# Kernel tuning notes

Measured on AMD Instinct MI355X. Metric: run time of the kernel, lower is better.

## Reference

```python
import jax, jax.numpy as jnp
import numpy as np

H = 32          # query heads
HKV = 8         # kv heads
HD = 128        # head dim
BS = 64         # sparse block size
LOCAL = 16      # local blocks
VERT = 8        # vertical stride
STEP = 1        # head sliding step = max(1, VERT // H) for non-homo heads
BASE = 1000000.0
ROPE_SCALE = 1.0
SCALE = 1.0 / np.sqrt(HD)


def setup_inputs() -> dict:
    key = jax.random.key(0)
    ks = jax.random.split(key, 6)
    T, D = 2048, H * HD
    std = 0.02
    return {
        'hidden_states': jax.random.normal(ks[0], (T, D), jnp.float32),
        'positions': jnp.arange(T, dtype=jnp.int32),
        'Wq': jax.random.normal(ks[1], (D, H * HD), jnp.float32) * std,
        'bq': jnp.zeros((H * HD,), jnp.float32),
        'Wk': jax.random.normal(ks[2], (D, HKV * HD), jnp.float32) * std,
        'bk': jnp.zeros((HKV * HD,), jnp.float32),
        'Wv': jax.random.normal(ks[3], (D, HKV * HD), jnp.float32) * std,
        'bv': jnp.zeros((HKV * HD,), jnp.float32),
        'Wo': jax.random.normal(ks[4], (D, D), jnp.float32) * std,
        'bo': jnp.zeros((D,), jnp.float32),
    }


def _rope_cos_sin(positions):
    # neox-style rotary, linear scaling (factor 1.0 -> identity)
    inv_freq = 1.0 / (BASE ** (jnp.arange(0, HD, 2, dtype=jnp.float32) / HD))  # [HD/2]
    t = positions.astype(jnp.float32) / ROPE_SCALE                             # [T]
    freqs = t[:, None] * inv_freq[None, :]                                     # [T, HD/2]
    return jnp.cos(freqs), jnp.sin(freqs)


def _apply_rope(x, cos, sin):
    # x: [T, h, HD], neox: rotate halves
    x1, x2 = x[..., : HD // 2], x[..., HD // 2 :]
    c, s = cos[:, None, :], sin[:, None, :]
    return jnp.concatenate([x1 * c - x2 * s, x2 * c + x1 * s], axis=-1)


def _block_sparse_mask(T):
    # per-head local + vertical-stride block pattern, causal at token level
    blk = jnp.arange(T) // BS
    qb, kb = blk[:, None], blk[None, :]                      # [T,T] block ids
    heads = jnp.arange(H)
    local = (qb - kb) < LOCAL                                # [T,T]
    vert = ((kb[None, :, :] + heads[:, None, None] * STEP + 1) % VERT) == 0  # [H,T,T]
    causal = jnp.arange(T)[:, None] >= jnp.arange(T)[None, :]
    return causal[None] & (local[None] | vert)               # [H,T,T] bool


def reference(hidden_states, positions, Wq, bq, Wk, bk, Wv, bv, Wo, bo):
    T = hidden_states.shape[0]
    q = (hidden_states @ Wq + bq).reshape(T, H, HD)
    k = (hidden_states @ Wk + bk).reshape(T, HKV, HD)
    v = (hidden_states @ Wv + bv).reshape(T, HKV, HD)

    cos, sin = _rope_cos_sin(positions)
    q = _apply_rope(q, cos, sin)
    k = _apply_rope(k, cos, sin)

    # GQA: repeat kv heads to match query heads
    k = jnp.repeat(k, H // HKV, axis=1)   # [T,H,HD]
    v = jnp.repeat(v, H // HKV, axis=1)

    scores = jnp.einsum('shd,thd->hst', q, k) * SCALE         # [H,T,T]
    mask = _block_sparse_mask(T)
    scores = jnp.where(mask, scores, jnp.finfo(scores.dtype).min)
    probs = jax.nn.softmax(scores, axis=-1)
    out = jnp.einsum('hst,thd->shd', probs, v).reshape(T, H * HD)
    return out @ Wo + bo
```

## Files before the change

### kernel.cpp

```cpp
#include <hip/hip_runtime.h>
#include <type_traits>

#define H_    32
#define HKV_  8
#define HD_   128
#define D_    4096
#define KVD_  1024
#define NQKV_ 6144

typedef __attribute__((ext_vector_type(8))) short s8v;
typedef __attribute__((ext_vector_type(4))) float f4v;

__device__ __forceinline__ float b2f(unsigned short u) {
  union { unsigned int i; float f; } v; v.i = ((unsigned int)u) << 16; return v.f;
}
__device__ __forceinline__ unsigned short f2b(float f) {
  unsigned int u = __float_as_uint(f);
  u += 0x7fffu + ((u >> 16) & 1u);
  return (unsigned short)(u >> 16);
}

__device__ __forceinline__ void gload16(const unsigned short* g, unsigned short* l) {
  __builtin_amdgcn_global_load_lds((const __attribute__((address_space(1))) void*)g,
                                   (__attribute__((address_space(3))) void*)l, 16, 0, 0);
}

__global__ void cvt_bf16(const float* __restrict__ x, unsigned short* __restrict__ y,
                         int n8)
{
  int i = blockIdx.x * blockDim.x + threadIdx.x;
  if (i >= n8) return;
  const float4* xp = (const float4*)x + (size_t)i * 2;
  float4 a = xp[0], b = xp[1];
  s8v v;
  v[0] = (short)f2b(a.x); v[1] = (short)f2b(a.y);
  v[2] = (short)f2b(a.z); v[3] = (short)f2b(a.w);
  v[4] = (short)f2b(b.x); v[5] = (short)f2b(b.y);
  v[6] = (short)f2b(b.z); v[7] = (short)f2b(b.w);
  *(s8v*)(y + (size_t)i * 8) = v;
}

__global__ void concat_bias(const float* __restrict__ bq, const float* __restrict__ bk,
                            const float* __restrict__ bv, float* __restrict__ o)
{
  int i = blockIdx.x * blockDim.x + threadIdx.x;
  float v = (i < D_) ? bq[i] : (i < D_ + KVD_) ? bk[i - D_] : bv[i - D_ - KVD_];
  o[i] = v;
}

__global__ __launch_bounds__(256) void cvt_transpose(
    const float* __restrict__ W, unsigned short* __restrict__ Wt, int K, int N)
{
  __shared__ unsigned short tile[64][72];
  const int k0 = blockIdx.y * 64, n0 = blockIdx.x * 64;
  const int tid = threadIdx.x;
#pragma unroll
  for (int it = 0; it < 4; ++it) {
    int idx = tid + it * 256;
    int r = idx >> 4;
    int c = (idx & 15) << 2;
    float4 w = *(const float4*)(W + (size_t)(k0 + r) * N + n0 + c);
    tile[c + 0][r] = f2b(w.x); tile[c + 1][r] = f2b(w.y);
    tile[c + 2][r] = f2b(w.z); tile[c + 3][r] = f2b(w.w);
  }
  __syncthreads();
#pragma unroll
  for (int it = 0; it < 2; ++it) {
    int idx = tid + it * 256;
    int n = idx >> 3;
    int kk = (idx & 7) << 3;
    *(s8v*)(Wt + (size_t)(n0 + n) * K + k0 + kk) = *(const s8v*)&tile[n][kk];
  }
}

__global__ __launch_bounds__(256) void vtrans(
    const unsigned short* __restrict__ S, int lds_, unsigned short* __restrict__ Dst,
    int T)
{
  __shared__ unsigned short tile[64][72];
  const int v0 = blockIdx.x * 64, t0 = blockIdx.y * 64;
  const int tid = threadIdx.x;
#pragma unroll
  for (int it = 0; it < 2; ++it) {
    int idx = tid + it * 256;
    int tr = idx >> 3;
    int vc = (idx & 7) << 3;
    s8v val = *(const s8v*)(S + (size_t)(t0 + tr) * lds_ + v0 + vc);
#pragma unroll
    for (int u = 0; u < 8; ++u) tile[vc + u][tr] = (unsigned short)val[u];
  }
  __syncthreads();
#pragma unroll
  for (int it = 0; it < 2; ++it) {
    int idx = tid + it * 256;
    int vr = idx >> 3;
    int tc = (idx & 7) << 3;
    *(s8v*)(Dst + (size_t)(v0 + vr) * T + t0 + tc) = *(const s8v*)&tile[vr][tc];
  }
}

template <typename OT>
__global__ __launch_bounds__(256) void gemm_bt(
    const unsigned short* __restrict__ A, const unsigned short* __restrict__ Bt,
    const float* __restrict__ bias, OT* __restrict__ C, int M, int N, int K, int ldc)
{
  __shared__ __align__(16) unsigned short As[128 * 32];
  __shared__ __align__(16) unsigned short Bs[128 * 32];

  const int tid  = threadIdx.x;
  const int wave = tid >> 6;
  const int lane = tid & 63;
  const int l16  = lane & 15;
  const int quad = lane >> 4;
  const int row0 = blockIdx.y * 128;
  const int col0 = blockIdx.x * 128;
  const int wr   = wave >> 1, wc = wave & 1;

  const int srow = lane >> 2;
  const int skk  = (lane & 3) << 3;
  const unsigned short* Ap = A  + (size_t)(row0 + wave * 32 + srow) * K + skk;
  const unsigned short* Bp = Bt + (size_t)(col0 + wave * 32 + srow) * K + skk;
  unsigned short* AsW = As + wave * 1024;
  unsigned short* BsW = Bs + wave * 1024;

  f4v acc[4][4] = {};

  for (int k0 = 0; k0 < K; k0 += 32) {
    __syncthreads();
    gload16(Ap,           AsW);
    gload16(Ap + 16 * K,  AsW + 512);
    gload16(Bp,           BsW);
    gload16(Bp + 16 * K,  BsW + 512);
    Ap += 32; Bp += 32;
    __syncthreads();

    s8v a[4], b[4];
#pragma unroll
    for (int i = 0; i < 4; ++i)
      a[i] = *(const s8v*)&As[(wr * 64 + i * 16 + l16) * 32 + quad * 8];
#pragma unroll
    for (int j = 0; j < 4; ++j)
      b[j] = *(const s8v*)&Bs[(wc * 64 + j * 16 + l16) * 32 + quad * 8];
#pragma unroll
    for (int i = 0; i < 4; ++i)
#pragma unroll
      for (int j = 0; j < 4; ++j)
        acc[i][j] = __builtin_amdgcn_mfma_f32_16x16x32_bf16(a[i], b[j], acc[i][j], 0, 0, 0);
  }

#pragma unroll
  for (int j = 0; j < 4; ++j) {
    int col = col0 + wc * 64 + j * 16 + l16;
    float bc = bias[col];
#pragma unroll
    for (int i = 0; i < 4; ++i) {
#pragma unroll
      for (int r = 0; r < 4; ++r) {
        int row = row0 + wr * 64 + i * 16 + quad * 4 + r;
        float o = acc[i][j][r] + bc;
        if constexpr (std::is_same_v<OT, float>) C[(size_t)row * ldc + col] = o;
        else                                     C[(size_t)row * ldc + col] = f2b(o);
      }
    }
  }
}

__global__ __launch_bounds__(256) void gemm_bt2(
    const unsigned short* __restrict__ A, const unsigned short* __restrict__ Bt,
    const float* __restrict__ bias, float* __restrict__ C, int M, int N, int K)
{
  __shared__ __align__(16) unsigned short As[128 * 32];
  __shared__ __align__(16) unsigned short Bs[64 * 32];

  const int tid  = threadIdx.x;
  const int wave = tid >> 6;
  const int lane = tid & 63;
  const int l16  = lane & 15;
  const int quad = lane >> 4;
  const int row0 = blockIdx.y * 128;
  const int col0 = blockIdx.x * 64;
  const int wr   = wave >> 1, wc = wave & 1;

  const int srow = lane >> 2;
  const int skk  = (lane & 3) << 3;
  const unsigned short* Ap = A  + (size_t)(row0 + wave * 32 + srow) * K + skk;
  const unsigned short* Bp = Bt + (size_t)(col0 + wave * 16 + srow) * K + skk;
  unsigned short* AsW = As + wave * 1024;
  unsigned short* BsW = Bs + wave * 512;

  f4v acc[4][2] = {};

  for (int k0 = 0; k0 < K; k0 += 32) {
    __syncthreads();
    gload16(Ap,           AsW);
    gload16(Ap + 16 * K,  AsW + 512);
    gload16(Bp,           BsW);
    Ap += 32; Bp += 32;
    __syncthreads();

    s8v a[4], b[2];
#pragma unroll
    for (int i = 0; i < 4; ++i)
      a[i] = *(const s8v*)&As[(wr * 64 + i * 16 + l16) * 32 + quad * 8];
#pragma unroll
    for (int j = 0; j < 2; ++j)
      b[j] = *(const s8v*)&Bs[(wc * 32 + j * 16 + l16) * 32 + quad * 8];
#pragma unroll
    for (int i = 0; i < 4; ++i)
#pragma unroll
      for (int j = 0; j < 2; ++j)
        acc[i][j] = __builtin_amdgcn_mfma_f32_16x16x32_bf16(a[i], b[j], acc[i][j], 0, 0, 0);
  }

#pragma unroll
  for (int j = 0; j < 2; ++j) {
    int col = col0 + wc * 32 + j * 16 + l16;
    float bc = bias[col];
#pragma unroll
    for (int i = 0; i < 4; ++i) {
#pragma unroll
      for (int r = 0; r < 4; ++r) {
        int row = row0 + wr * 64 + i * 16 + quad * 4 + r;
        C[(size_t)row * N + col] = acc[i][j][r] + bc;
      }
    }
  }
}

__global__ void sincos_tab(const int* __restrict__ pos, float* __restrict__ ct,
                           float* __restrict__ st)
{
  const int t = blockIdx.x, d = threadIdx.x;
  float inv = powf(1.0e6f, -(float)d * (1.0f / 64.0f));
  float fr  = (float)pos[t] * inv;
  float s, c;
  sincosf(fr, &s, &c);
  ct[t * 64 + d] = c;
  st[t * 64 + d] = s;
}

__global__ void rope_apply(unsigned short* __restrict__ qkv,
                           const float* __restrict__ ct, const float* __restrict__ st,
                           int T)
{
  const int t  = blockIdx.x;
  const int hh = blockIdx.y;
  const int d  = threadIdx.x;
  unsigned short* p = qkv + (size_t)t * NQKV_ + hh * HD_;
  const float g = (hh < H_) ? (0.08838834764831845f * 1.4426950408889634f) : 1.0f;
  float c = ct[t * 64 + d], s = st[t * 64 + d];
  float x1 = b2f(p[d]), x2 = b2f(p[d + 64]);
  p[d]      = f2b((x1 * c - x2 * s) * g);
  p[d + 64] = f2b((x2 * c + x1 * s) * g);
}

__global__ __launch_bounds__(256) void attn_sparse(
    const unsigned short* __restrict__ QKV, int ldq,
    const unsigned short* __restrict__ Vt, unsigned short* __restrict__ O, int T)
{
  __shared__ __align__(16) unsigned short lds[16384];
  unsigned short* ldsK = lds;
  unsigned short* ldsV = lds + 8192;
  unsigned short* ldsP = lds;

  const int h    = blockIdx.x;
  const int qb   = (gridDim.y - 1) - blockIdx.y;
  const int hkv  = h >> 2;
  const int tid  = threadIdx.x;
  const int wave = tid >> 6;
  const int lane = tid & 63;
  const int l16  = lane & 15;
  const int quad = lane >> 4;

  const int qrow = qb * 64 + wave * 16 + l16;
  s8v qf[4];
#pragma unroll
  for (int s = 0; s < 4; ++s)
    qf[s] = *(const s8v*)(QKV + (size_t)qrow * ldq + h * HD_ + s * 32 + quad * 8);

  const int lr4 = lane >> 2;
  const int lc8 = (lane & 3) << 3;
  const unsigned short* Kp0 = QKV + (size_t)(wave * 16 + lr4) * ldq
                              + D_ + hkv * HD_ + lc8;
  unsigned short* Kd0 = ldsK + wave * 512;
  const unsigned short* Vp0 = Vt + (size_t)(hkv * HD_ + wave * 32 + lr4) * T + lc8;
  unsigned short* Vd0 = ldsV + wave * 1024;

  float mrow[4] = {-1e30f, -1e30f, -1e30f, -1e30f};
  float lrow[4] = {0.f, 0.f, 0.f, 0.f};
  f4v oacc[8] = {};
  const int rowinb = wave * 16 + quad * 4;

  for (int kb = 0; kb <= qb; ++kb) {
    if (!((qb - kb < 16) || (((kb + h + 1) & 7) == 0))) continue;

    __syncthreads();
    {
      const unsigned short* kp = Kp0 + (size_t)(kb * 64) * ldq;
      const unsigned short* vp = Vp0 + kb * 64;
#pragma unroll
      for (int t = 0; t < 4; ++t)
        gload16(kp + t * 32, Kd0 + t * 2048);
#pragma unroll
      for (int t = 0; t < 4; ++t)
        gload16(vp + (size_t)((t >> 1) * 16) * T + (t & 1) * 32,
                Vd0 + (t & 1) * 4096 + (t >> 1) * 512);
    }
    __syncthreads();

    f4v sacc[4] = {};
#pragma unroll
    for (int kt = 0; kt < 4; ++kt) {
#pragma unroll
      for (int s = 0; s < 4; ++s) {
        s8v b = *(const s8v*)&ldsK[s * 2048 + (kt * 16 + l16) * 32 + quad * 8];
        sacc[kt] = __builtin_amdgcn_mfma_f32_16x16x32_bf16(qf[s], b, sacc[kt], 0, 0, 0);
      }
    }
    __syncthreads();

    const bool diag = (kb == qb);
    float p[4][4];
#pragma unroll
    for (int r = 0; r < 4; ++r) {
      float mx = -1e30f;
#pragma unroll
      for (int kt = 0; kt < 4; ++kt) {
        float sc = sacc[kt][r];
        if (diag && (kt * 16 + l16 > rowinb + r)) sc = -1e30f;
        p[r][kt] = sc;
        mx = fmaxf(mx, sc);
      }
#pragma unroll
      for (int off = 1; off < 16; off <<= 1)
        mx = fmaxf(mx, __shfl_xor(mx, off));
      float newm = fmaxf(mrow[r], mx);
      float alpha = exp2f(mrow[r] - newm);
      mrow[r] = newm;
      float rs = 0.f;
#pragma unroll
      for (int kt = 0; kt < 4; ++kt) {
        unsigned short pb = f2b(exp2f(p[r][kt] - newm));
        ldsP[wave * 1152 + (quad * 4 + r) * 72 + kt * 16 + l16] = pb;
        rs += b2f(pb);
      }
#pragma unroll
      for (int off = 1; off < 16; off <<= 1)
        rs += __shfl_xor(rs, off);
      lrow[r] = lrow[r] * alpha + rs;
#pragma unroll
      for (int dt = 0; dt < 8; ++dt) oacc[dt][r] *= alpha;
    }

#pragma unroll
    for (int s2 = 0; s2 < 2; ++s2) {
      s8v af = *(const s8v*)&ldsP[wave * 1152 + l16 * 72 + s2 * 32 + quad * 8];
#pragma unroll
      for (int dt = 0; dt < 8; ++dt) {
        s8v vf = *(const s8v*)&ldsV[s2 * 4096 + (dt * 16 + l16) * 32 + quad * 8];
        oacc[dt] = __builtin_amdgcn_mfma_f32_16x16x32_bf16(af, vf, oacc[dt], 0, 0, 0);
      }
    }
  }

#pragma unroll
  for (int r = 0; r < 4; ++r) {
    float inv = 1.0f / lrow[r];
    size_t rowoff = (size_t)(qb * 64 + rowinb + r) * D_ + h * HD_;
#pragma unroll
    for (int dt = 0; dt < 8; ++dt)
      O[rowoff + dt * 16 + l16] = f2b(oacc[dt][r] * inv);
  }
}

extern "C" void kernel_launch(void* const* d_in, const int* in_sizes, int n_in,
                              void* d_out, int out_size, void* d_ws, size_t ws_size,
                              hipStream_t stream)
{
  const float* hs  = (const float*)d_in[0];
  const int*   pos = (const int*)d_in[1];
  const float* Wq  = (const float*)d_in[2];
  const float* bq  = (const float*)d_in[3];
  const float* Wk  = (const float*)d_in[4];
  const float* bk  = (const float*)d_in[5];
  const float* Wv  = (const float*)d_in[6];
  const float* bv  = (const float*)d_in[7];
  const float* Wo  = (const float*)d_in[8];
  const float* bo  = (const float*)d_in[9];
  float* out = (float*)d_out;

  const int T = in_sizes[1];

  const size_t nQ = (size_t)T * D_;
  unsigned short* hsb  = (unsigned short*)d_ws;
  unsigned short* qkv  = hsb + nQ;
  unsigned short* vt   = qkv + (size_t)T * NQKV_;
  unsigned short* wbuf = vt  + (size_t)KVD_ * T;
  unsigned short* tail = wbuf + (size_t)NQKV_ * D_;
  float* bqkv = (float*)tail;
  float* ct   = bqkv + NQKV_;
  float* st   = ct + (size_t)T * 64;
  unsigned short* abuf = hsb;

  dim3 blk(256);
  cvt_bf16<<<dim3((int)(nQ / 8 / 256)), blk, 0, stream>>>(hs, hsb, (int)(nQ / 8));
  concat_bias<<<dim3(NQKV_ / 256), blk, 0, stream>>>(bq, bk, bv, bqkv);
  sincos_tab<<<dim3(T), dim3(64), 0, stream>>>(pos, ct, st);

  cvt_transpose<<<dim3(D_ / 64,   D_ / 64), blk, 0, stream>>>(Wq, wbuf, D_, D_);
  cvt_transpose<<<dim3(KVD_ / 64, D_ / 64), blk, 0, stream>>>(
      Wk, wbuf + (size_t)D_ * D_, D_, KVD_);
  cvt_transpose<<<dim3(KVD_ / 64, D_ / 64), blk, 0, stream>>>(
      Wv, wbuf + (size_t)(D_ + KVD_) * D_, D_, KVD_);

  gemm_bt<unsigned short><<<dim3(NQKV_ / 128, T / 128), blk, 0, stream>>>(
      hsb, wbuf, bqkv, qkv, T, NQKV_, D_, NQKV_);

  rope_apply<<<dim3(T, H_ + HKV_), dim3(64), 0, stream>>>(qkv, ct, st, T);
  vtrans<<<dim3(KVD_ / 64, T / 64), blk, 0, stream>>>(
      qkv + D_ + KVD_, NQKV_, vt, T);

  attn_sparse<<<dim3(H_, T / 64), blk, 0, stream>>>(qkv, NQKV_, vt, abuf, T);

  cvt_transpose<<<dim3(D_ / 64, D_ / 64), blk, 0, stream>>>(Wo, wbuf, D_, D_);
  gemm_bt2<<<dim3(D_ / 64, T / 128), blk, 0, stream>>>(
      abuf, wbuf, bo, out, T, D_, D_);
}
```

Baseline: 552.7 us.

## Rewrite QKV GEMM with 256x256 tiles and a 4-stage swizzled LDS pipeline

Replaces the 128x128, 4-wave QKV projection GEMM with a 512-thread kernel that computes 256x256 output tiles. It prefetches three K-tiles ahead through a 4-buffer LDS ring using direct global-to-LDS loads and explicit vmcnt waits. LDS rows are XOR-swizzled to reduce bank conflicts. MFMA bursts run at raised wave priority, and a block-index remap groups neighbouring tiles onto the same XCD. The goal is more data reuse per byte loaded and load latency hidden behind compute. In exchange it launches only 192 workgroups using 128 KB of LDS each, so fewer blocks than CUs will run at once.

```diff
diff --git a/kernel.cpp b/kernel.cpp
--- a/kernel.cpp
+++ b/kernel.cpp
@@ -100,66 +100,112 @@
 }
 
 template <typename OT>
-__global__ __launch_bounds__(256) void gemm_bt(
+__global__ __launch_bounds__(512, 2) void gemm_bt8(
     const unsigned short* __restrict__ A, const unsigned short* __restrict__ Bt,
-    const float* __restrict__ bias, OT* __restrict__ C, int M, int N, int K, int ldc)
-{
-  __shared__ __align__(16) unsigned short As[128 * 32];
-  __shared__ __align__(16) unsigned short Bs[128 * 32];
+    const float* __restrict__ bias, OT* __restrict__ C,
+    int M, int N, int K, int ldc)
+{
+  __shared__ __align__(16) unsigned short lds[65536];
 
   const int tid  = threadIdx.x;
   const int wave = tid >> 6;
   const int lane = tid & 63;
   const int l16  = lane & 15;
   const int quad = lane >> 4;
-  const int row0 = blockIdx.y * 128;
-  const int col0 = blockIdx.x * 128;
-  const int wr   = wave >> 1, wc = wave & 1;
+  const int wm   = wave >> 2;
+  const int wn   = wave & 3;
+
+  const int nbx = N >> 8;
+  const int nwg = nbx * (M >> 8);
+  int bid = blockIdx.x;
+  if ((nwg & 7) == 0) bid = (bid & 7) * (nwg >> 3) + (bid >> 3);
+  const int row0 = (bid / nbx) << 8;
+  const int col0 = (bid % nbx) << 8;
 
   const int srow = lane >> 2;
-  const int skk  = (lane & 3) << 3;
-  const unsigned short* Ap = A  + (size_t)(row0 + wave * 32 + srow) * K + skk;
-  const unsigned short* Bp = Bt + (size_t)(col0 + wave * 32 + srow) * K + skk;
-  unsigned short* AsW = As + wave * 1024;
-  unsigned short* BsW = Bs + wave * 1024;
-
-  f4v acc[4][4] = {};
-
-  for (int k0 = 0; k0 < K; k0 += 32) {
-    __syncthreads();
-    gload16(Ap,           AsW);
-    gload16(Ap + 16 * K,  AsW + 512);
-    gload16(Bp,           BsW);
-    gload16(Bp + 16 * K,  BsW + 512);
-    Ap += 32; Bp += 32;
-    __syncthreads();
-
-    s8v a[4], b[4];
-#pragma unroll
-    for (int i = 0; i < 4; ++i)
-      a[i] = *(const s8v*)&As[(wr * 64 + i * 16 + l16) * 32 + quad * 8];
-#pragma unroll
-    for (int j = 0; j < 4; ++j)
-      b[j] = *(const s8v*)&Bs[(wc * 64 + j * 16 + l16) * 32 + quad * 8];
+  const int scol = ((lane & 3) ^ (srow & 3)) << 3;
+  const unsigned short* Ap0 = A  + (size_t)(row0 + wave * 32 + srow) * K + scol;
+  const unsigned short* Bp0 = Bt + (size_t)(col0 + wave * 32 + srow) * K + scol;
+
+  auto STAGE_A = [&](int tile) {
+    unsigned short* d = lds + (tile & 3) * 8192 + wave * 1024;
+    const unsigned short* s = Ap0 + (size_t)tile * 32;
+    gload16(s, d);
+    gload16(s + 16 * (size_t)K, d + 512);
+  };
+  auto STAGE_B = [&](int tile) {
+    unsigned short* d = lds + 32768 + (tile & 3) * 8192 + wave * 1024;
+    const unsigned short* s = Bp0 + (size_t)tile * 32;
+    gload16(s, d);
+    gload16(s + 16 * (size_t)K, d + 512);
+  };
+
+  const int slot = ((quad ^ (l16 & 3)) << 3);
+  const int aoff = (wm * 128 + l16) * 32 + slot;
+  const int boff = (wn * 64  + l16) * 32 + slot;
+
+  f4v acc[8][4] = {};
+  const int nt = K >> 5;
+
+  STAGE_A(0); STAGE_B(0);
+  STAGE_A(1); STAGE_B(1);
+  STAGE_A(2); STAGE_B(2);
+  asm volatile("s_waitcnt vmcnt(8)" ::: "memory");
+  __builtin_amdgcn_s_barrier();
+
+  for (int t = 0; t < nt; ++t) {
+    const unsigned short* Ab = lds + (t & 3) * 8192;
+    const unsigned short* Bb = lds + 32768 + (t & 3) * 8192;
+    s8v a[8], b[4];
+
+    if (t + 3 < nt) STAGE_A(t + 3);
+#pragma unroll
+    for (int i = 0; i < 4; ++i) a[i] = *(const s8v*)&Ab[aoff + i * 512];
+#pragma unroll
+    for (int j = 0; j < 4; ++j) b[j] = *(const s8v*)&Bb[boff + j * 512];
+    __builtin_amdgcn_s_barrier();
+    asm volatile("s_waitcnt lgkmcnt(0)" ::: "memory");
+    __builtin_amdgcn_sched_barrier(0);
+    __builtin_amdgcn_s_setprio(1);
 #pragma unroll
     for (int i = 0; i < 4; ++i)
 #pragma unroll
       for (int j = 0; j < 4; ++j)
         acc[i][j] = __builtin_amdgcn_mfma_f32_16x16x32_bf16(a[i], b[j], acc[i][j], 0, 0, 0);
+    __builtin_amdgcn_s_setprio(0);
+    __builtin_amdgcn_s_barrier();
+
+    if (t + 3 < nt) STAGE_B(t + 3);
+#pragma unroll
+    for (int i = 0; i < 4; ++i) a[4 + i] = *(const s8v*)&Ab[aoff + (4 + i) * 512];
+    __builtin_amdgcn_s_barrier();
+    asm volatile("s_waitcnt lgkmcnt(0)" ::: "memory");
+    __builtin_amdgcn_sched_barrier(0);
+    __builtin_amdgcn_s_setprio(1);
+#pragma unroll
+    for (int i = 0; i < 4; ++i)
+#pragma unroll
+      for (int j = 0; j < 4; ++j)
+        acc[4 + i][j] = __builtin_amdgcn_mfma_f32_16x16x32_bf16(a[4 + i], b[j], acc[4 + i][j], 0, 0, 0);
+    __builtin_amdgcn_s_setprio(0);
+    if (t < nt - 3)       { asm volatile("s_waitcnt vmcnt(8)" ::: "memory"); }
+    else if (t == nt - 3) { asm volatile("s_waitcnt vmcnt(4)" ::: "memory"); }
+    else if (t == nt - 2) { asm volatile("s_waitcnt vmcnt(0)" ::: "memory"); }
+    __builtin_amdgcn_s_barrier();
   }
 
 #pragma unroll
   for (int j = 0; j < 4; ++j) {
-    int col = col0 + wc * 64 + j * 16 + l16;
-    float bc = bias[col];
-#pragma unroll
-    for (int i = 0; i < 4; ++i) {
+    const int col = col0 + wn * 64 + j * 16 + l16;
+    const float bc = bias[col];
+#pragma unroll
+    for (int i = 0; i < 8; ++i) {
+      const int rowb = row0 + wm * 128 + i * 16 + quad * 4;
 #pragma unroll
       for (int r = 0; r < 4; ++r) {
-        int row = row0 + wr * 64 + i * 16 + quad * 4 + r;
         float o = acc[i][j][r] + bc;
-        if constexpr (std::is_same_v<OT, float>) C[(size_t)row * ldc + col] = o;
-        else                                     C[(size_t)row * ldc + col] = f2b(o);
+        if constexpr (std::is_same_v<OT, float>) C[(size_t)(rowb + r) * ldc + col] = o;
+        else                                     C[(size_t)(rowb + r) * ldc + col] = f2b(o);
       }
     }
   }
@@ -413,7 +459,7 @@
   cvt_transpose<<<dim3(KVD_ / 64, D_ / 64), blk, 0, stream>>>(
       Wv, wbuf + (size_t)(D_ + KVD_) * D_, D_, KVD_);
 
-  gemm_bt<unsigned short><<<dim3(NQKV_ / 128, T / 128), blk, 0, stream>>>(
+  gemm_bt8<unsigned short><<<dim3((NQKV_ / 256) * (T / 256)), dim3(512), 0, stream>>>(
       hsb, wbuf, bqkv, qkv, T, NQKV_, D_, NQKV_);
 
   rope_apply<<<dim3(T, H_ + HKV_), dim3(64), 0, stream>>>(qkv, ct, st, T);
```

Result: no change. 560.7 us (+1.4%).
